# Kernel tuning notes

Measured on AMD Instinct MI355X. Metric: run time of the kernel, lower is better.

The kernel has to match this reference:

```python
import jax, jax.numpy as jnp
import numpy as np

N_NODES = 50000
N_EDGES = 625000
IN_C, HID_C, OUT_C = 128, 128, 64


def _glorot(key, shape):
    lim = float(np.sqrt(6.0 / (shape[0] + shape[1])))
    return jax.random.uniform(key, shape, jnp.float32, -lim, lim)


def setup_inputs() -> dict:
    key = jax.random.key(0)
    ks = jax.random.split(key, 8)
    x = jax.random.normal(ks[0], (N_NODES, IN_C), jnp.float32)
    edge_index = jax.random.randint(ks[1], (2, N_EDGES), 0, N_NODES, jnp.int32)
    dims = [(IN_C, HID_C), (HID_C, HID_C), (HID_C, OUT_C)]
    params = {}
    for i, (di, do) in enumerate(dims, start=1):
        k1, k2 = jax.random.split(ks[1 + i])
        params[f"Wl{i}"] = _glorot(k1, (di, do))  # neighbor (lin_l) weight
        params[f"Wr{i}"] = _glorot(k2, (di, do))  # root (lin_r) weight
        params[f"b{i}"] = jnp.zeros((do,), jnp.float32)
    return {"x": x, "edge_index": edge_index, **params}


def _segment_mean(msg, dst, n):
    s = jax.ops.segment_sum(msg, dst, num_segments=n)
    cnt = jax.ops.segment_sum(jnp.ones(dst.shape, msg.dtype), dst, num_segments=n)
    return s / jnp.maximum(cnt, 1.0)[:, None]


def _sage_conv(x, src, dst, Wl, Wr, b):
    # mean-aggregate source features at destinations, then lin_l(agg)+lin_r(x)
    agg = _segment_mean(x[src], dst, x.shape[0])  # [N, d_in]
    return agg @ Wl + x @ Wr + b


def reference(x, edge_index, Wl1, Wr1, b1, Wl2, Wr2, b2, Wl3, Wr3, b3):
    src, dst = edge_index[0], edge_index[1]
    h = jax.nn.relu(_sage_conv(x, src, dst, Wl1, Wr1, b1))
    # dropout is identity in eval mode
    h = jax.nn.relu(_sage_conv(h, src, dst, Wl2, Wr2, b2))
    out = _sage_conv(h, src, dst, Wl3, Wr3, b3)
    return out
```

## Files before the change

kernel.cpp:

```cpp
#include <hip/hip_runtime.h>

#define NN 50000
#define NE 625000
#define CAP 64

typedef __bf16 bf16_8 __attribute__((ext_vector_type(8)));
typedef __bf16 bf16_4 __attribute__((ext_vector_type(4)));
typedef float f32_4 __attribute__((ext_vector_type(4)));
typedef float f32_2 __attribute__((ext_vector_type(2)));


__device__ __forceinline__ void convw_one(const float* Wl, const float* Wr,
                                          __bf16* Wt, int NO, int i) {
    int k = i & 127;
    int n = i >> 7;
    const float* W = (n < NO) ? Wl : Wr;
    int nn = (n < NO) ? n : n - NO;
    Wt[i] = (__bf16)W[k * NO + nn];
}

__global__ void init_kernel(int* __restrict__ deg,
                            const float* __restrict__ Wl1, const float* __restrict__ Wr1, __bf16* __restrict__ Wt1,
                            const float* __restrict__ Wl2, const float* __restrict__ Wr2, __bf16* __restrict__ Wt2,
                            const float* __restrict__ Wl3, const float* __restrict__ Wr3, __bf16* __restrict__ Wt3) {
    int i = blockIdx.x * blockDim.x + threadIdx.x;
    if (i < NN) deg[i] = 0;
    if (i < 32768)      convw_one(Wl1, Wr1, Wt1, 128, i);
    else if (i < 65536) convw_one(Wl2, Wr2, Wt2, 128, i - 32768);
    else if (i < 81920) convw_one(Wl3, Wr3, Wt3, 64, i - 65536);
}


__global__ void fill2_kernel(const int* __restrict__ src, const int* __restrict__ dst,
                             int* __restrict__ deg, int* __restrict__ col2, int e) {
    int i = blockIdx.x * blockDim.x + threadIdx.x;
    if (i < e) {
        int d = dst[i];
        int slot = atomicAdd(&deg[d], 1);
        if (slot < CAP) col2[d * CAP + slot] = src[i];
    }
}


template<int MODE, int ZF32, int NFRAG, int YF8>
__global__ __launch_bounds__(256, 6)
void fused_layer(const void* __restrict__ Asrc, const __bf16* __restrict__ zprev,
                 const int* __restrict__ deg, const int* __restrict__ col2,
                 const __bf16* __restrict__ Bt, const float* __restrict__ bias,
                 void* __restrict__ Yp, void* __restrict__ Zp) {
    __shared__ __bf16 As[32 * 128];
    const int t = threadIdx.x;
    const int m0 = blockIdx.x * 32;
    const int NO = NFRAG * 32;

    if (MODE == 0) {
        const float* x = (const float*)Asrc;
        #pragma unroll
        for (int it = 0; it < 2; ++it) {
            int r = (t >> 4) + it * 16;
            int c = t & 15;
            int gm = m0 + r;
            float4 lo = make_float4(0.f, 0.f, 0.f, 0.f), hi = lo;
            if (gm < NN) {
                lo = *(const float4*)&x[(size_t)gm * 128 + c * 8];
                hi = *(const float4*)&x[(size_t)gm * 128 + c * 8 + 4];
            }
            bf16_8 v;
            v[0] = (__bf16)lo.x; v[1] = (__bf16)lo.y; v[2] = (__bf16)lo.z; v[3] = (__bf16)lo.w;
            v[4] = (__bf16)hi.x; v[5] = (__bf16)hi.y; v[6] = (__bf16)hi.z; v[7] = (__bf16)hi.w;
            *(bf16_8*)&As[r * 128 + (c ^ (r & 7)) * 8] = v;
        }
    } else {
        const unsigned char* yp = (const unsigned char*)Asrc;
        int g = t >> 4, s = t & 15;
        #pragma unroll
        for (int ni = 0; ni < 2; ++ni) {
            int rl = g + ni * 16;
            int node = m0 + rl;
            bf16_8 o = {};
            if (node < NN) {
                int dg = deg[node];
                int nedge = min(dg, CAP);
                float iv = 1.0f / (float)max(dg, 1);
                const int* cl = &col2[node * CAP];
                float acc[8] = {};
                for (int e0 = 0; e0 < nedge; e0 += 8) {
                    int us[8];
                    #pragma unroll
                    for (int k = 0; k < 8; ++k) {
                        int ec = min(e0 + k, nedge - 1);
                        us[k] = cl[ec];
                    }
                    uint2 vv[8];
                    #pragma unroll
                    for (int k = 0; k < 8; ++k)
                        vv[k] = *(const uint2*)&yp[(size_t)us[k] * 128 + s * 8];
                    #pragma unroll
                    for (int k = 0; k < 8; ++k) {
                        float wk = (e0 + k < nedge) ? 1.0f : 0.0f;
                        f32_2 a0 = __builtin_amdgcn_cvt_pk_f32_fp8(vv[k].x, false);
                        f32_2 a1 = __builtin_amdgcn_cvt_pk_f32_fp8(vv[k].x, true);
                        f32_2 a2 = __builtin_amdgcn_cvt_pk_f32_fp8(vv[k].y, false);
                        f32_2 a3 = __builtin_amdgcn_cvt_pk_f32_fp8(vv[k].y, true);
                        acc[0] += wk * a0.x; acc[1] += wk * a0.y;
                        acc[2] += wk * a1.x; acc[3] += wk * a1.y;
                        acc[4] += wk * a2.x; acc[5] += wk * a2.y;
                        acc[6] += wk * a3.x; acc[7] += wk * a3.y;
                    }
                }
                bf16_8 zv = *(const bf16_8*)&zprev[(size_t)node * 128 + s * 8];
                #pragma unroll
                for (int j = 0; j < 8; ++j) {
                    float v = acc[j] * iv + (float)zv[j];
                    o[j] = (__bf16)fmaxf(v, 0.f);
                }
            }
            *(bf16_8*)&As[rl * 128 + (s ^ (rl & 7)) * 8] = o;
        }
    }
    __syncthreads();

    const int w = t >> 6;
    const int wn = w * 16 * NFRAG;
    const int lane = t & 63;
    const int lr = lane & 15;
    const int kg = lane >> 4;

    f32_4 acc[2][NFRAG] = {};
    #pragma unroll
    for (int ks = 0; ks < 4; ++ks) {
        int kc16 = ks * 4 + kg;
        bf16_8 a[2], bb[NFRAG];
        #pragma unroll
        for (int mi = 0; mi < 2; ++mi) {
            int r = mi * 16 + lr;
            a[mi] = *(const bf16_8*)&As[r * 128 + (kc16 ^ (r & 7)) * 8];
        }
        #pragma unroll
        for (int ni = 0; ni < NFRAG; ++ni) {
            int n = wn + ni * 16 + lr;
            bb[ni] = *(const bf16_8*)&Bt[(size_t)n * 128 + kc16 * 8];
        }
        #pragma unroll
        for (int mi = 0; mi < 2; ++mi)
            #pragma unroll
            for (int ni = 0; ni < NFRAG; ++ni)
                acc[mi][ni] = __builtin_amdgcn_mfma_f32_16x16x32_bf16(a[mi], bb[ni], acc[mi][ni], 0, 0, 0);
    }

    #pragma unroll
    for (int mi = 0; mi < 2; ++mi) {
        int gmb = m0 + mi * 16 + kg * 4;
        #pragma unroll
        for (int ni = 0; ni < NFRAG; ++ni) {
            int gc = wn + ni * 16 + lr;
            bool isY = gc < NO;
            float bv = 0.f;
            if (!isY) bv = bias[gc - NO];
            #pragma unroll
            for (int rr = 0; rr < 4; ++rr) {
                int gm = gmb + rr;
                if (gm < NN) {
                    float vv = acc[mi][ni][rr] + bv;
                    if (isY) {
                        if (YF8) {
                            int pk = __builtin_amdgcn_cvt_pk_fp8_f32(vv, vv, 0, false);
                            ((unsigned char*)Yp)[(size_t)gm * NO + gc] = (unsigned char)(pk & 0xff);
                        } else {
                            ((__bf16*)Yp)[(size_t)gm * NO + gc] = (__bf16)vv;
                        }
                    }
                    else if (ZF32) ((float*)Zp)[(size_t)gm * NO + (gc - NO)] = vv;
                    else ((__bf16*)Zp)[(size_t)gm * NO + (gc - NO)] = (__bf16)vv;
                }
            }
        }
    }
}


__global__ __launch_bounds__(256, 6)
void agg64_kernel(const __bf16* __restrict__ y, const float* __restrict__ z,
                  const int* __restrict__ deg, const int* __restrict__ col2,
                  float* __restrict__ fout, int n) {
    int gid = blockIdx.x * 16 + (threadIdx.x >> 4);
    if (gid >= n) return;
    int s = threadIdx.x & 15;
    int dg = deg[gid];
    int nedge = min(dg, CAP);
    float iv = 1.0f / (float)max(dg, 1);
    const int* cl = &col2[gid * CAP];
    float acc[4] = {};
    for (int e0 = 0; e0 < nedge; e0 += 8) {
        int us[8];
        #pragma unroll
        for (int k = 0; k < 8; ++k) {
            int ec = min(e0 + k, nedge - 1);
            us[k] = cl[ec];
        }
        bf16_4 vv[8];
        #pragma unroll
        for (int k = 0; k < 8; ++k)
            vv[k] = *(const bf16_4*)&y[(size_t)us[k] * 64 + s * 4];
        #pragma unroll
        for (int k = 0; k < 8; ++k) {
            float wk = (e0 + k < nedge) ? 1.0f : 0.0f;
            acc[0] += wk * (float)vv[k][0];
            acc[1] += wk * (float)vv[k][1];
            acc[2] += wk * (float)vv[k][2];
            acc[3] += wk * (float)vv[k][3];
        }
    }
    float4 zv = *(const float4*)&z[(size_t)gid * 64 + s * 4];
    float4 o;
    o.x = acc[0] * iv + zv.x;
    o.y = acc[1] * iv + zv.y;
    o.z = acc[2] * iv + zv.z;
    o.w = acc[3] * iv + zv.w;
    *(float4*)&fout[(size_t)gid * 64 + s * 4] = o;
}


extern "C" void kernel_launch(void* const* d_in, const int* in_sizes, int n_in,
                              void* d_out, int out_size, void* d_ws, size_t ws_size,
                              hipStream_t stream) {
    const float* x   = (const float*)d_in[0];
    const int*   ei  = (const int*)d_in[1];
    const int*   src = ei;
    const int*   dst = ei + NE;
    const float* Wl1 = (const float*)d_in[2];
    const float* Wr1 = (const float*)d_in[3];
    const float* b1  = (const float*)d_in[4];
    const float* Wl2 = (const float*)d_in[5];
    const float* Wr2 = (const float*)d_in[6];
    const float* b2  = (const float*)d_in[7];
    const float* Wl3 = (const float*)d_in[8];
    const float* Wr3 = (const float*)d_in[9];
    const float* b3  = (const float*)d_in[10];
    float* out = (float*)d_out;

    char* ws = (char*)d_ws;
    size_t off = 0;
    auto alloc = [&](size_t bytes) -> void* {
        void* p = ws + off;
        off += (bytes + 255) & ~(size_t)255;
        return p;
    };

    int*    deg      = (int*)alloc(NN * 4);
    int*    col2     = (int*)alloc((size_t)NN * CAP * 4);
    unsigned char* y1 = (unsigned char*)alloc((size_t)NN * 128);
    __bf16* z1       = (__bf16*)alloc((size_t)NN * 128 * 2);
    unsigned char* y2 = (unsigned char*)alloc((size_t)NN * 128);
    __bf16* z2       = (__bf16*)alloc((size_t)NN * 128 * 2);
    __bf16* y3       = (__bf16*)alloc((size_t)NN * 64 * 2);
    float*  zf       = (float*)alloc((size_t)NN * 64 * 4);
    __bf16* Wt1      = (__bf16*)alloc(256 * 128 * 2);
    __bf16* Wt2      = (__bf16*)alloc(256 * 128 * 2);
    __bf16* Wt3      = (__bf16*)alloc(128 * 128 * 2);

    init_kernel<<<320, 256, 0, stream>>>(deg, Wl1, Wr1, Wt1, Wl2, Wr2, Wt2, Wl3, Wr3, Wt3);
    fill2_kernel<<<(NE + 255) / 256, 256, 0, stream>>>(src, dst, deg, col2, NE);

    int fblocks = (NN + 31) / 32;
    int aggBlocks = (NN + 15) / 16;

    fused_layer<0, 0, 4, 1><<<fblocks, 256, 0, stream>>>(x, nullptr, nullptr, nullptr,
                                                         Wt1, b1, y1, z1);
    fused_layer<1, 0, 4, 1><<<fblocks, 256, 0, stream>>>(y1, z1, deg, col2,
                                                         Wt2, b2, y2, z2);
    fused_layer<1, 1, 2, 0><<<fblocks, 256, 0, stream>>>(y2, z2, deg, col2,
                                                         Wt3, b3, y3, zf);
    agg64_kernel<<<aggBlocks, 256, 0, stream>>>(y3, zf, deg, col2, out, NN);
}
```

Measured before the change: 143.6 us.

## Fuse adjacency bucket fill into layer-1 GEMM kernel and co-locate degree with neighbor list

Removes the separate fill kernel by giving every fourth block of the first layer's kernel the job of scattering edges into per-node buckets, while the other blocks run the layer-1 dense transform concurrently. The degree counter now sits in slot 0 of each 64-int bucket row, so the aggregation reads degree and neighbor list from one cache line region, and CAP drops to 63 to fit. This saves a launch and overlaps the atomic-heavy CSR build with GEMM work. The cost is contention between the two roles within one grid and a block mapping that depends on hardcoded grid constants.

```diff
diff --git a/kernel.cpp b/kernel.cpp
--- a/kernel.cpp
+++ b/kernel.cpp
@@ -2,7 +2,11 @@
 
 #define NN 50000
 #define NE 625000
-#define CAP 64
+#define CAP 63
+#define BSTR 64
+#define L1B 1563
+#define FILLB 521
+#define GRID1 2084
 
 typedef __bf16 bf16_8 __attribute__((ext_vector_type(8)));
 typedef __bf16 bf16_4 __attribute__((ext_vector_type(4)));
@@ -19,39 +23,43 @@
     Wt[i] = (__bf16)W[k * NO + nn];
 }
 
-__global__ void init_kernel(int* __restrict__ deg,
+__global__ void init_kernel(int* __restrict__ bucket,
                             const float* __restrict__ Wl1, const float* __restrict__ Wr1, __bf16* __restrict__ Wt1,
                             const float* __restrict__ Wl2, const float* __restrict__ Wr2, __bf16* __restrict__ Wt2,
                             const float* __restrict__ Wl3, const float* __restrict__ Wr3, __bf16* __restrict__ Wt3) {
     int i = blockIdx.x * blockDim.x + threadIdx.x;
-    if (i < NN) deg[i] = 0;
+    if (i < NN) bucket[(size_t)i * BSTR] = 0;
     if (i < 32768)      convw_one(Wl1, Wr1, Wt1, 128, i);
     else if (i < 65536) convw_one(Wl2, Wr2, Wt2, 128, i - 32768);
     else if (i < 81920) convw_one(Wl3, Wr3, Wt3, 64, i - 65536);
 }
 
 
-__global__ void fill2_kernel(const int* __restrict__ src, const int* __restrict__ dst,
-                             int* __restrict__ deg, int* __restrict__ col2, int e) {
-    int i = blockIdx.x * blockDim.x + threadIdx.x;
-    if (i < e) {
-        int d = dst[i];
-        int slot = atomicAdd(&deg[d], 1);
-        if (slot < CAP) col2[d * CAP + slot] = src[i];
-    }
-}
-
-
 template<int MODE, int ZF32, int NFRAG, int YF8>
 __global__ __launch_bounds__(256, 6)
 void fused_layer(const void* __restrict__ Asrc, const __bf16* __restrict__ zprev,
-                 const int* __restrict__ deg, const int* __restrict__ col2,
-                 const __bf16* __restrict__ Bt, const float* __restrict__ bias,
-                 void* __restrict__ Yp, void* __restrict__ Zp) {
+                 int* __restrict__ bucket, const __bf16* __restrict__ Bt,
+                 const float* __restrict__ bias, void* __restrict__ Yp,
+                 void* __restrict__ Zp,
+                 const int* __restrict__ esrc, const int* __restrict__ edst) {
     __shared__ __bf16 As[32 * 128];
     const int t = threadIdx.x;
-    const int m0 = blockIdx.x * 32;
     const int NO = NFRAG * 32;
+
+    int bid = blockIdx.x;
+    if (MODE == 0) {
+        if ((bid & 3) == 3) {
+            int ft = (bid >> 2) * 256 + t;
+            for (int i = ft; i < NE; i += FILLB * 256) {
+                int d = edst[i];
+                int slot = atomicAdd(&bucket[(size_t)d * BSTR], 1);
+                if (slot < CAP) bucket[(size_t)d * BSTR + 1 + slot] = esrc[i];
+            }
+            return;
+        }
+        bid = bid - (bid >> 2);
+    }
+    const int m0 = bid * 32;
 
     if (MODE == 0) {
         const float* x = (const float*)Asrc;
@@ -79,10 +87,11 @@
             int node = m0 + rl;
             bf16_8 o = {};
             if (node < NN) {
-                int dg = deg[node];
+                const int* bk = &bucket[(size_t)node * BSTR];
+                int dg = bk[0];
                 int nedge = min(dg, CAP);
                 float iv = 1.0f / (float)max(dg, 1);
-                const int* cl = &col2[node * CAP];
+                const int* cl = bk + 1;
                 float acc[8] = {};
                 for (int e0 = 0; e0 < nedge; e0 += 8) {
                     int us[8];
@@ -181,15 +190,15 @@
 
 __global__ __launch_bounds__(256, 6)
 void agg64_kernel(const __bf16* __restrict__ y, const float* __restrict__ z,
-                  const int* __restrict__ deg, const int* __restrict__ col2,
-                  float* __restrict__ fout, int n) {
+                  const int* __restrict__ bucket, float* __restrict__ fout, int n) {
     int gid = blockIdx.x * 16 + (threadIdx.x >> 4);
     if (gid >= n) return;
     int s = threadIdx.x & 15;
-    int dg = deg[gid];
+    const int* bk = &bucket[(size_t)gid * BSTR];
+    int dg = bk[0];
     int nedge = min(dg, CAP);
     float iv = 1.0f / (float)max(dg, 1);
-    const int* cl = &col2[gid * CAP];
+    const int* cl = bk + 1;
     float acc[4] = {};
     for (int e0 = 0; e0 < nedge; e0 += 8) {
         int us[8];
@@ -247,8 +256,7 @@
         return p;
     };
 
-    int*    deg      = (int*)alloc(NN * 4);
-    int*    col2     = (int*)alloc((size_t)NN * CAP * 4);
+    int*    bucket   = (int*)alloc((size_t)NN * BSTR * 4);
     unsigned char* y1 = (unsigned char*)alloc((size_t)NN * 128);
     __bf16* z1       = (__bf16*)alloc((size_t)NN * 128 * 2);
     unsigned char* y2 = (unsigned char*)alloc((size_t)NN * 128);
@@ -259,17 +267,15 @@
     __bf16* Wt2      = (__bf16*)alloc(256 * 128 * 2);
     __bf16* Wt3      = (__bf16*)alloc(128 * 128 * 2);
 
-    init_kernel<<<320, 256, 0, stream>>>(deg, Wl1, Wr1, Wt1, Wl2, Wr2, Wt2, Wl3, Wr3, Wt3);
-    fill2_kernel<<<(NE + 255) / 256, 256, 0, stream>>>(src, dst, deg, col2, NE);
-
-    int fblocks = (NN + 31) / 32;
+    init_kernel<<<320, 256, 0, stream>>>(bucket, Wl1, Wr1, Wt1, Wl2, Wr2, Wt2, Wl3, Wr3, Wt3);
+
     int aggBlocks = (NN + 15) / 16;
 
-    fused_layer<0, 0, 4, 1><<<fblocks, 256, 0, stream>>>(x, nullptr, nullptr, nullptr,
-                                                         Wt1, b1, y1, z1);
-    fused_layer<1, 0, 4, 1><<<fblocks, 256, 0, stream>>>(y1, z1, deg, col2,
-                                                         Wt2, b2, y2, z2);
-    fused_layer<1, 1, 2, 0><<<fblocks, 256, 0, stream>>>(y2, z2, deg, col2,
-                                                         Wt3, b3, y3, zf);
-    agg64_kernel<<<aggBlocks, 256, 0, stream>>>(y3, zf, deg, col2, out, NN);
-}
+    fused_layer<0, 0, 4, 1><<<GRID1, 256, 0, stream>>>(x, nullptr, bucket,
+                                                       Wt1, b1, y1, z1, src, dst);
+    fused_layer<1, 0, 4, 1><<<L1B, 256, 0, stream>>>(y1, z1, bucket,
+                                                     Wt2, b2, y2, z2, nullptr, nullptr);
+    fused_layer<1, 1, 2, 0><<<L1B, 256, 0, stream>>>(y2, z2, bucket,
+                                                     Wt3, b3, y3, zf, nullptr, nullptr);
+    agg64_kernel<<<aggBlocks, 256, 0, stream>>>(y3, zf, bucket, out, NN);
+}
```

Measured after the change: 201.5 us. +40.3%, slower.
